# Kernel tuning notes

Hardware: AMD Instinct MI355X
Metric: run time of the kernel (lower is better)

## Reference

```python
import jax, jax.numpy as jnp
import numpy as np

N_HEAD = 8
HIDDEN = 512
EPS_LN = 1e-3  # keras LayerNormalization default epsilon


def layernorm(x, gamma, beta, eps=EPS_LN):
    mu = jnp.mean(x, axis=-1, keepdims=True)
    var = jnp.mean((x - mu) ** 2, axis=-1, keepdims=True)
    return (x - mu) * jax.lax.rsqrt(var + eps) * gamma + beta


def setup_inputs() -> dict:
    key = jax.random.key(0)
    ks = jax.random.split(key, 10)
    bs, NE, F = 512, 128, HIDDEN
    x = jax.random.normal(ks[0], (bs, NE, F), dtype=jnp.float32)
    mask = (jax.random.uniform(ks[1], (bs, 1, NE)) < 0.85).astype(jnp.float32)
    # guarantee at least one live entity per row
    mask = mask.at[:, :, 0].set(1.0)
    s = 1.0 / np.sqrt(F)
    Wqk = jax.random.normal(ks[2], (F, 2 * HIDDEN), dtype=jnp.float32) * s
    bqk = jnp.zeros((2 * HIDDEN,), jnp.float32)
    Wv = jax.random.normal(ks[3], (F, HIDDEN), dtype=jnp.float32) * s
    bv = jnp.zeros((HIDDEN,), jnp.float32)
    Wmlp = jax.random.normal(ks[4], (F, HIDDEN), dtype=jnp.float32) * s
    bmlp = jnp.zeros((HIDDEN,), jnp.float32)
    g_pre = jnp.ones((F,), jnp.float32)
    b_pre = jnp.zeros((F,), jnp.float32)
    g_post = jnp.ones((F,), jnp.float32)
    b_post = jnp.zeros((F,), jnp.float32)
    return dict(x=x, mask=mask, Wqk=Wqk, bqk=bqk, Wv=Wv, bv=bv,
                Wmlp=Wmlp, bmlp=bmlp, g_pre=g_pre, b_pre=b_pre,
                g_post=g_post, b_post=b_post)


def reference(x, mask, Wqk, bqk, Wv, bv, Wmlp, bmlp, g_pre, b_pre, g_post, b_post):
    bs, NE, F = x.shape
    h, d = N_HEAD, HIDDEN // N_HEAD
    x4 = x[:, None]  # (bs, 1, NE, F)

    # pre-norm only feeds qkv projections; residual uses raw x4
    inp = layernorm(x4, g_pre, b_pre)

    qk = (inp @ Wqk + bqk).reshape(bs, 1, NE, h, d, 2)
    q, k = qk[..., 0], qk[..., 1]                       # (bs,1,NE,h,d)
    v = (inp @ Wv + bv).reshape(bs, 1, NE, h, d)

    logits = jnp.einsum('btnhd,btmhd->bthnm', q, k) / np.sqrt(d)  # (bs,1,h,NE,NE)

    m5 = mask[:, :, None, None, :]                      # (bs,1,1,1,NE)
    logits = logits - (1.0 - m5) * 1e10
    logits = logits - jnp.max(logits, axis=-1, keepdims=True)
    un = jnp.exp(logits) * m5
    p = un / (jnp.sum(un, axis=-1, keepdims=True) + 1e-10)
    p = p * m5

    att = jnp.einsum('bthnm,btmhd->btnhd', p, v).reshape(bs, 1, NE, HIDDEN)
    a = att @ Wmlp + bmlp                               # mlp_layer=1, no activation
    y = x4 + a                                          # residual
    y = layernorm(y, g_post, b_post)

    # masked average pooling over entities
    mE = mask[..., None]                                # (bs,1,NE,1)
    pooled = jnp.sum(y * mE, axis=-2) / (jnp.sum(mE, axis=-2) + 1e-5)  # (bs,1,F)
    return pooled.reshape(bs, F)
```

## Files before the change

kernel.cpp:

```cpp
#include <hip/hip_runtime.h>
#include <hip/hip_bf16.h>


typedef __bf16 bf16;
typedef __bf16 bf16x8 __attribute__((ext_vector_type(8)));
typedef __bf16 bf16x4 __attribute__((ext_vector_type(4)));
typedef float f32x4 __attribute__((ext_vector_type(4)));

__device__ __forceinline__ f32x4 mfma16(bf16x8 a, bf16x8 b, f32x4 c) {
    return __builtin_amdgcn_mfma_f32_16x16x32_bf16(a, b, c, 0, 0, 0);
}

typedef const unsigned int __attribute__((address_space(1)))* gptr_t;
typedef unsigned int __attribute__((address_space(3)))* lptr_t;
__device__ __forceinline__ void gld16(const void* g, void* l) {
    __builtin_amdgcn_global_load_lds((gptr_t)g, (lptr_t)l, 16, 0, 0);
}

#define SWZ(byteoff, row) ((byteoff) ^ (((row) & 7) << 4))


__global__ __launch_bounds__(256) void prep_split_kernel(
    const float* __restrict__ Wqk, const float* __restrict__ bqk,
    const float* __restrict__ Wv, const float* __restrict__ bv,
    const float* __restrict__ Wmlp,
    bf16* __restrict__ Wqkv_s, bf16* __restrict__ Wmlp_s, float* __restrict__ bQKV)
{
    int t = blockIdx.x * 256 + threadIdx.x;
    if (t < 524288) {
        int k = t >> 10, c = t & 1023;
        int h = c >> 7, w7 = c & 127, d = w7 >> 1, isK = w7 & 1;
        int n = isK * 512 + h * 64 + d;
        int tn = n >> 7, nc = n & 127, kc = k >> 6, kw = k & 63;
        Wqkv_s[((size_t)(tn * 8 + kc) * 128 + nc) * 64 + kw] = (bf16)Wqk[t];
    } else if (t < 786432) {
        int u = t - 524288;
        int k = u >> 9, c = u & 511;
        int n = 1024 + c;
        int tn = n >> 7, nc = n & 127, kc = k >> 6, kw = k & 63;
        Wqkv_s[((size_t)(tn * 8 + kc) * 128 + nc) * 64 + kw] = (bf16)Wv[u];
    } else if (t < 1048576) {
        int u = t - 786432;
        int k = u >> 9, c = u & 511;
        int chunk = k >> 5, kw = k & 31;
        Wmlp_s[chunk * 16384 + c * 32 + (kw ^ ((c & 3) << 3))] = (bf16)Wmlp[u];
    } else if (t < 1050112) {
        int j = t - 1048576;
        int region = j >> 9, w9 = j & 511, h = w9 >> 6, d = w9 & 63;
        float v;
        if (region == 0)      v = bqk[h * 128 + d * 2];
        else if (region == 1) v = bqk[h * 128 + d * 2 + 1];
        else                  v = bv[h * 64 + d];
        bQKV[j] = v;
    }
}

__global__ __launch_bounds__(256) void ln_kernel(
    const float* __restrict__ x, const float* __restrict__ g,
    const float* __restrict__ b, bf16* __restrict__ inp)
{
    int row = blockIdx.x * 4 + (threadIdx.x >> 6);
    int lane = threadIdx.x & 63;
    int k0 = lane * 8;
    const float* xr = x + (size_t)row * 512 + k0;
    f32x4 a0 = *(const f32x4*)xr;
    f32x4 a1 = *(const f32x4*)(xr + 4);
    float s = 0.f, ss = 0.f;
#pragma unroll
    for (int i = 0; i < 4; i++) {
        s += a0[i] + a1[i];
        ss += a0[i] * a0[i] + a1[i] * a1[i];
    }
#pragma unroll
    for (int m = 1; m < 64; m <<= 1) {
        s  += __shfl_xor(s, m, 64);
        ss += __shfl_xor(ss, m, 64);
    }
    float mu = s * (1.f / 512.f);
    float rstd = rsqrtf(ss * (1.f / 512.f) - mu * mu + 1e-3f);
    f32x4 g0 = *(const f32x4*)(g + k0);
    f32x4 g1 = *(const f32x4*)(g + k0 + 4);
    f32x4 b0 = *(const f32x4*)(b + k0);
    f32x4 b1 = *(const f32x4*)(b + k0 + 4);
    bf16x8 ov;
#pragma unroll
    for (int i = 0; i < 4; i++) {
        ov[i]     = (bf16)((a0[i] - mu) * rstd * g0[i] + b0[i]);
        ov[i + 4] = (bf16)((a1[i] - mu) * rstd * g1[i] + b1[i]);
    }
    *(bf16x8*)(inp + (size_t)row * 512 + k0) = ov;
}

__global__ __launch_bounds__(256) void qkv_gemm_kernel(
    const bf16* __restrict__ inp, const bf16* __restrict__ Wqkv_s,
    const float* __restrict__ bQKV,
    bf16* __restrict__ q, bf16* __restrict__ kbuf, bf16* __restrict__ vt)
{
    __shared__ __align__(16) bf16 As[128 * 64];
    __shared__ __align__(16) bf16 Bs[128 * 64];
    const int bid = blockIdx.x;
    const int idx = (bid & 7) * 768 + (bid >> 3);
    const int tm = idx / 12, tn = idx % 12;
    const int tid = threadIdx.x;
    const int w = tid >> 6, l = tid & 63;
    const int wr = w >> 1, wc = w & 1;
    const int l15 = l & 15, l4 = l >> 4;

    const f32x4 fz = {0.f, 0.f, 0.f, 0.f};
    f32x4 acc[4][4];
#pragma unroll
    for (int m = 0; m < 4; m++)
#pragma unroll
        for (int n = 0; n < 4; n++) acc[m][n] = fz;

    const int arow = l >> 3;
    const int axc = ((l & 7) ^ arow) * 8;
    const bf16* Abase = inp + (size_t)(tm * 128) * 512;
    const int rsw = (l15 & 7) << 4;

    for (int kc = 0; kc < 8; kc++) {
#pragma unroll
        for (int i = 0; i < 4; i++) {
            int rg = (i * 4 + w) * 8;
            gld16(Abase + (size_t)(rg + arow) * 512 + kc * 64 + axc,
                  As + (i * 4 + w) * 512);
        }
        const bf16* Bbase = Wqkv_s + (size_t)(tn * 8 + kc) * 8192;
#pragma unroll
        for (int i = 0; i < 4; i++) {
            gld16(Bbase + (size_t)((i * 4 + w) * 8 + arow) * 64 + axc,
                  Bs + (i * 4 + w) * 512);
        }
        __syncthreads();
#pragma unroll
        for (int kk = 0; kk < 2; kk++) {
            const int kb = (kk * 64 + l4 * 16) ^ rsw;
            bf16x8 af[4], bfr[4];
#pragma unroll
            for (int m = 0; m < 4; m++)
                af[m] = *(const bf16x8*)((const char*)As + (wr * 64 + m * 16 + l15) * 128 + kb);
#pragma unroll
            for (int n = 0; n < 4; n++)
                bfr[n] = *(const bf16x8*)((const char*)Bs + (wc * 64 + n * 16 + l15) * 128 + kb);
#pragma unroll
            for (int m = 0; m < 4; m++)
#pragma unroll
                for (int n = 0; n < 4; n++)
                    acc[m][n] = mfma16(af[m], bfr[n], acc[m][n]);
        }
        __syncthreads();
    }

    const int colBase = tn * 128 + wc * 64;
    const int mrowBase = tm * 128 + wr * 64;
#pragma unroll
    for (int n = 0; n < 4; n++) {
        int col = colBase + n * 16 + l15;
        float bias = bQKV[col];
        int within = col & 511, hh = within >> 6, dd = within & 63;
#pragma unroll
        for (int m = 0; m < 4; m++) {
            int mr0 = mrowBase + m * 16 + l4 * 4;
            int bb = mr0 >> 7, e0 = mr0 & 127;
            size_t base = (size_t)(bb * 8 + hh) * 8192;
            if (tn < 4) {
#pragma unroll
                for (int r = 0; r < 4; r++)
                    q[base + (size_t)(e0 + r) * 64 + dd] = (bf16)(acc[m][n][r] + bias);
            } else if (tn < 8) {
#pragma unroll
                for (int r = 0; r < 4; r++) {
                    int e = e0 + r;
                    kbuf[base + (size_t)e * 64 + (dd ^ ((e & 7) << 3))] = (bf16)(acc[m][n][r] + bias);
                }
            } else {
                bf16x4 pk;
#pragma unroll
                for (int r = 0; r < 4; r++) pk[r] = (bf16)(acc[m][n][r] + bias);
                *(bf16x4*)(vt + base + (size_t)dd * 128 + (e0 ^ ((dd & 7) << 3))) = pk;
            }
        }
    }
}

__global__ __launch_bounds__(512) void attn_split_kernel(
    const bf16* __restrict__ q, const bf16* __restrict__ kbuf,
    const bf16* __restrict__ vt, const float* __restrict__ mask,
    bf16* __restrict__ att)
{
    __shared__ __align__(16) char Ks[128 * 128];
    __shared__ __align__(16) char VTs[64 * 256];
    __shared__ __align__(16) char Ps[128 * 256];
    __shared__ float mrow[128];

    const int bid = blockIdx.x;
    const int b = bid & 511, h = bid >> 9;
    const size_t bh = (size_t)(b * 8 + h);
    const int tid = threadIdx.x;
    const int w = tid >> 6, l = tid & 63;
    const int l15 = l & 15, l4 = l >> 4, R0 = w * 16;

    const bf16* kb = kbuf + bh * 8192;
    const bf16* vb = vt + bh * 8192;
#pragma unroll
    for (int i = 0; i < 2; i++) {
        gld16(kb + ((i * 8 + w) * 64 + l) * 8, (bf16*)Ks + (i * 8 + w) * 512);
        gld16(vb + ((i * 8 + w) * 64 + l) * 8, (bf16*)VTs + (i * 8 + w) * 512);
    }
    if (tid < 128) mrow[tid] = mask[b * 128 + tid];
    __syncthreads();

    const f32x4 fz = {0.f, 0.f, 0.f, 0.f};
    const bf16* qp = q + bh * 8192 + (size_t)(R0 + l15) * 64 + l4 * 8;
    bf16x8 af0 = *(const bf16x8*)(qp);
    bf16x8 af1 = *(const bf16x8*)(qp + 32);
    f32x4 accL[8];
#pragma unroll
    for (int n = 0; n < 8; n++) accL[n] = fz;
#pragma unroll
    for (int ks = 0; ks < 2; ks++) {
        bf16x8 af = ks ? af1 : af0;
        int k2 = (ks * 32 + l4 * 8) * 2;
#pragma unroll
        for (int nt = 0; nt < 8; nt++) {
            int krow = nt * 16 + l15;
            bf16x8 bfr = *(const bf16x8*)(Ks + krow * 128 + (k2 ^ ((krow & 7) << 4)));
            accL[nt] = mfma16(af, bfr, accL[nt]);
        }
    }
    float pv[32];
#pragma unroll
    for (int r = 0; r < 4; r++) {
        float mx = -1e30f;
#pragma unroll
        for (int nt = 0; nt < 8; nt++) {
            int colk = nt * 16 + l15;
            float v = accL[nt][r] * 0.125f - (1.0f - mrow[colk]) * 1e10f;
            pv[nt * 4 + r] = v;
            mx = fmaxf(mx, v);
        }
#pragma unroll
        for (int m = 1; m < 16; m <<= 1) mx = fmaxf(mx, __shfl_xor(mx, m, 64));
        float sum = 0.f;
#pragma unroll
        for (int nt = 0; nt < 8; nt++) {
            int colk = nt * 16 + l15;
            float e = __expf(pv[nt * 4 + r] - mx) * mrow[colk];
            pv[nt * 4 + r] = e;
            sum += e;
        }
#pragma unroll
        for (int m = 1; m < 16; m <<= 1) sum += __shfl_xor(sum, m, 64);
        float inv = 1.0f / (sum + 1e-10f);
        int prow = R0 + l4 * 4 + r;
#pragma unroll
        for (int nt = 0; nt < 8; nt++) {
            bf16 pb = (bf16)(pv[nt * 4 + r] * inv);
            *(bf16*)(Ps + prow * 256 + SWZ((nt * 16 + l15) * 2, prow)) = pb;
        }
    }
    __syncthreads();

    f32x4 accO[4];
#pragma unroll
    for (int n = 0; n < 4; n++) accO[n] = fz;
#pragma unroll
    for (int ks = 0; ks < 4; ks++) {
        int k2 = (ks * 32 + l4 * 8) * 2;
        int prow = R0 + l15;
        bf16x8 af = *(const bf16x8*)(Ps + prow * 256 + (k2 ^ ((prow & 7) << 4)));
#pragma unroll
        for (int nt = 0; nt < 4; nt++) {
            int d = nt * 16 + l15;
            bf16x8 bfr = *(const bf16x8*)(VTs + d * 256 + (k2 ^ ((d & 7) << 4)));
            accO[nt] = mfma16(af, bfr, accO[nt]);
        }
    }
    bf16* outp = att + (size_t)(b * 128) * 512 + h * 64;
#pragma unroll
    for (int nt = 0; nt < 4; nt++) {
        int d = nt * 16 + l15;
#pragma unroll
        for (int r = 0; r < 4; r++) {
            int e = R0 + l4 * 4 + r;
            outp[(size_t)e * 512 + d] = (bf16)accO[nt][r];
        }
    }
}

__global__ __launch_bounds__(512) void mlp_split_kernel(
    const bf16* __restrict__ att, const bf16* __restrict__ Wmlp_s,
    const float* __restrict__ bmlp, const float* __restrict__ x,
    const float* __restrict__ mask, const float* __restrict__ gpost,
    const float* __restrict__ bpost, float* __restrict__ out)
{
    __shared__ __align__(16) bf16 Bs[2][512 * 32];
    __shared__ float pool[512];
    __shared__ float gb[1024];
    __shared__ float mrow[128];
    __shared__ float msum_s;

    const int b = blockIdx.x;
    const int tid = threadIdx.x;
    const int w = tid >> 6, l = tid & 63;
    const int l15 = l & 15, l4 = l >> 4;
    const int R0 = w * 16;

    pool[tid] = 0.f;
    gb[tid] = gpost[tid];
    gb[512 + tid] = bpost[tid];
    if (tid < 128) mrow[tid] = mask[b * 128 + tid];

#pragma unroll
    for (int i = 0; i < 4; i++)
        gld16(Wmlp_s + ((i * 8 + w) * 64 + l) * 8, &Bs[0][(i * 8 + w) * 512]);
    __syncthreads();
    if (w == 0) {
        float v = mrow[l] + mrow[64 + l];
#pragma unroll
        for (int m = 1; m < 64; m <<= 1) v += __shfl_xor(v, m, 64);
        if (l == 0) msum_s = v;
    }

    const f32x4 fz = {0.f, 0.f, 0.f, 0.f};
    f32x4 acc[32];
#pragma unroll
    for (int n = 0; n < 32; n++) acc[n] = fz;
    const bf16* Ab = att + (size_t)(b * 128 + R0 + l15) * 512 + l4 * 8;
    int cur = 0;
    for (int ks = 0; ks < 16; ks++) {
        if (ks < 15) {
            const bf16* src = Wmlp_s + (ks + 1) * 16384;
#pragma unroll
            for (int i = 0; i < 4; i++)
                gld16(src + ((i * 8 + w) * 64 + l) * 8, &Bs[cur ^ 1][(i * 8 + w) * 512]);
        }
        bf16x8 af = *(const bf16x8*)(Ab + ks * 32);
#pragma unroll
        for (int nt = 0; nt < 32; nt++) {
            int ncol = nt * 16 + l15;
            bf16x8 bfr = *(const bf16x8*)((const char*)&Bs[cur][0] + ncol * 64 + ((l4 * 16) ^ ((ncol & 3) << 4)));
            acc[nt] = mfma16(af, bfr, acc[nt]);
        }
        __syncthreads();
        cur ^= 1;
    }
#pragma unroll
    for (int nt = 0; nt < 32; nt++) {
        int col = nt * 16 + l15;
        float bb = bmlp[col];
#pragma unroll
        for (int r = 0; r < 4; r++) {
            int row = R0 + l4 * 4 + r;
            acc[nt][r] = acc[nt][r] + bb + x[((size_t)b * 128 + row) * 512 + col];
        }
    }
    float mu[4], rs[4];
#pragma unroll
    for (int r = 0; r < 4; r++) {
        float s = 0.f, ss = 0.f;
#pragma unroll
        for (int nt = 0; nt < 32; nt++) {
            float v = acc[nt][r];
            s += v; ss += v * v;
        }
#pragma unroll
        for (int m = 1; m < 16; m <<= 1) {
            s  += __shfl_xor(s, m, 64);
            ss += __shfl_xor(ss, m, 64);
        }
        float m_ = s * (1.f / 512.f);
        mu[r] = m_;
        rs[r] = rsqrtf(ss * (1.f / 512.f) - m_ * m_ + 1e-3f);
    }
#pragma unroll
    for (int nt = 0; nt < 32; nt++) {
        int col = nt * 16 + l15;
        float g = gb[col], bb = gb[512 + col];
        float s = 0.f;
#pragma unroll
        for (int r = 0; r < 4; r++) {
            int row = R0 + l4 * 4 + r;
            float y = (acc[nt][r] - mu[r]) * rs[r] * g + bb;
            s += y * mrow[row];
        }
        atomicAdd(&pool[col], s);
    }
    __syncthreads();
    out[(size_t)b * 512 + tid] = pool[tid] / (msum_s + 1e-5f);
}

__global__ __launch_bounds__(256) void prep_kernel(
    const float* __restrict__ Wqk, const float* __restrict__ bqk,
    const float* __restrict__ Wv, const float* __restrict__ bv,
    const float* __restrict__ Wmlp,
    bf16* __restrict__ Wqkv_t, bf16* __restrict__ Wmlp_t, float* __restrict__ bQKV)
{
    int t = blockIdx.x * 256 + threadIdx.x;
    const int NQKV = 8 * 192 * 512;
    if (t < NQKV) {
        int h = t / (192 * 512);
        int rem = t - h * (192 * 512);
        int n = rem >> 9;
        int k = rem & 511;
        float v;
        if (n < 64)       v = Wqk[k * 1024 + h * 128 + n * 2];
        else if (n < 128) v = Wqk[k * 1024 + h * 128 + (n - 64) * 2 + 1];
        else              v = Wv[k * 512 + h * 64 + (n - 128)];
        Wqkv_t[t] = (bf16)v;
    } else {
        int u = t - NQKV;
        if (u < 512 * 512) {
            int col = u >> 9, k = u & 511;
            Wmlp_t[u] = (bf16)Wmlp[k * 512 + col];
        } else {
            int j = u - 512 * 512;
            if (j < 1536) {
                int h = j / 192, n = j - h * 192;
                float v;
                if (n < 64)       v = bqk[h * 128 + n * 2];
                else if (n < 128) v = bqk[h * 128 + (n - 64) * 2 + 1];
                else              v = bv[h * 64 + (n - 128)];
                bQKV[j] = v;
            }
        }
    }
}

__global__ __launch_bounds__(512) void attn_kernel(
    const bf16* __restrict__ inp, const float* __restrict__ mask,
    const bf16* __restrict__ Wqkv_t, const float* __restrict__ bQKV,
    bf16* __restrict__ att)
{
    __shared__ __align__(16) char Qs[128 * 128];
    __shared__ __align__(16) char Ks[128 * 128];
    __shared__ __align__(16) char VTs[64 * 256];
    __shared__ __align__(16) char Ps[128 * 256];
    __shared__ float mrow[128];

    const int bid = blockIdx.x;
    const int b = bid & 511;
    const int h = bid >> 9;
    const int tid = threadIdx.x;
    const int w = tid >> 6, l = tid & 63;
    const int l15 = l & 15, l4 = l >> 4;
    const int R0 = w * 16;

    if (tid < 128) mrow[tid] = mask[b * 128 + tid];

    const bf16* A  = inp + (size_t)(b * 128) * 512;
    const bf16* Wh = Wqkv_t + (size_t)h * 192 * 512;
    const f32x4 fz = {0.f, 0.f, 0.f, 0.f};

    f32x4 acc[12];
#pragma unroll
    for (int n = 0; n < 12; n++) acc[n] = fz;
    const bf16* aptr = A + (size_t)(R0 + l15) * 512 + l4 * 8;
#pragma unroll 4
    for (int ks = 0; ks < 16; ks++) {
        bf16x8 af = *(const bf16x8*)(aptr + ks * 32);
#pragma unroll
        for (int n = 0; n < 12; n++) {
            bf16x8 bfr = *(const bf16x8*)(Wh + (size_t)(n * 16 + l15) * 512 + ks * 32 + l4 * 8);
            acc[n] = mfma16(af, bfr, acc[n]);
        }
    }
#pragma unroll
    for (int n = 0; n < 12; n++) {
        int col = n * 16 + l15;
        float bias = bQKV[h * 192 + col];
#pragma unroll
        for (int r = 0; r < 4; r++) {
            int row = R0 + l4 * 4 + r;
            bf16 val = (bf16)(acc[n][r] + bias);
            if (n < 4) {
                *(bf16*)(Qs + row * 128 + SWZ(col * 2, row)) = val;
            } else if (n < 8) {
                *(bf16*)(Ks + row * 128 + SWZ((col - 64) * 2, row)) = val;
            } else {
                int d = col - 128;
                *(bf16*)(VTs + d * 256 + SWZ(row * 2, d)) = val;
            }
        }
    }
    __syncthreads();

    f32x4 accL[8];
#pragma unroll
    for (int n = 0; n < 8; n++) accL[n] = fz;
#pragma unroll
    for (int ks = 0; ks < 2; ks++) {
        int k = ks * 32 + l4 * 8;
        int qrow = R0 + l15;
        bf16x8 af = *(const bf16x8*)(Qs + qrow * 128 + SWZ(k * 2, qrow));
#pragma unroll
        for (int nt = 0; nt < 8; nt++) {
            int krow = nt * 16 + l15;
            bf16x8 bfr = *(const bf16x8*)(Ks + krow * 128 + SWZ(k * 2, krow));
            accL[nt] = mfma16(af, bfr, accL[nt]);
        }
    }
    float pv[32];
#pragma unroll
    for (int r = 0; r < 4; r++) {
        float mx = -1e30f;
#pragma unroll
        for (int nt = 0; nt < 8; nt++) {
            int colk = nt * 16 + l15;
            float v = accL[nt][r] * 0.125f - (1.0f - mrow[colk]) * 1e10f;
            pv[nt * 4 + r] = v;
            mx = fmaxf(mx, v);
        }
#pragma unroll
        for (int m = 1; m < 16; m <<= 1) mx = fmaxf(mx, __shfl_xor(mx, m, 64));
        float sum = 0.f;
#pragma unroll
        for (int nt = 0; nt < 8; nt++) {
            int colk = nt * 16 + l15;
            float e = __expf(pv[nt * 4 + r] - mx) * mrow[colk];
            pv[nt * 4 + r] = e;
            sum += e;
        }
#pragma unroll
        for (int m = 1; m < 16; m <<= 1) sum += __shfl_xor(sum, m, 64);
        float inv = 1.0f / (sum + 1e-10f);
        int prow = R0 + l4 * 4 + r;
#pragma unroll
        for (int nt = 0; nt < 8; nt++) {
            bf16 pb = (bf16)(pv[nt * 4 + r] * inv);
            *(bf16*)(Ps + prow * 256 + SWZ((nt * 16 + l15) * 2, prow)) = pb;
        }
    }
    __syncthreads();

    f32x4 accO[4];
#pragma unroll
    for (int n = 0; n < 4; n++) accO[n] = fz;
#pragma unroll
    for (int ks = 0; ks < 4; ks++) {
        int k = ks * 32 + l4 * 8;
        int prow = R0 + l15;
        bf16x8 af = *(const bf16x8*)(Ps + prow * 256 + SWZ(k * 2, prow));
#pragma unroll
        for (int nt = 0; nt < 4; nt++) {
            int d = nt * 16 + l15;
            bf16x8 bfr = *(const bf16x8*)(VTs + d * 256 + SWZ(k * 2, d));
            accO[nt] = mfma16(af, bfr, accO[nt]);
        }
    }
    bf16* outp = att + (size_t)(b * 128) * 512 + h * 64;
#pragma unroll
    for (int nt = 0; nt < 4; nt++) {
        int d = nt * 16 + l15;
#pragma unroll
        for (int r = 0; r < 4; r++) {
            int e = R0 + l4 * 4 + r;
            outp[(size_t)e * 512 + d] = (bf16)accO[nt][r];
        }
    }
}

__global__ __launch_bounds__(512) void mlp_kernel(
    const bf16* __restrict__ att, const bf16* __restrict__ Wmlp_t,
    const float* __restrict__ bmlp, const float* __restrict__ x,
    const float* __restrict__ mask, const float* __restrict__ gpost,
    const float* __restrict__ bpost, float* __restrict__ out)
{
    __shared__ float pool[512];
    __shared__ float gb[1024];
    __shared__ float mrow[128];
    __shared__ float msum_s;

    const int b = blockIdx.x;
    const int tid = threadIdx.x;
    const int w = tid >> 6, l = tid & 63;
    const int l15 = l & 15, l4 = l >> 4;
    const int R0 = w * 16;

    pool[tid] = 0.f;
    gb[tid] = gpost[tid];
    gb[512 + tid] = bpost[tid];
    if (tid < 128) mrow[tid] = mask[b * 128 + tid];
    __syncthreads();
    if (w == 0) {
        float v = mrow[l] + mrow[64 + l];
#pragma unroll
        for (int m = 1; m < 64; m <<= 1) v += __shfl_xor(v, m, 64);
        if (l == 0) msum_s = v;
    }

    const f32x4 fz = {0.f, 0.f, 0.f, 0.f};
    f32x4 acc[32];
#pragma unroll
    for (int n = 0; n < 32; n++) acc[n] = fz;
    const bf16* Ab = att + (size_t)(b * 128 + R0 + l15) * 512 + l4 * 8;
#pragma unroll 2
    for (int ks = 0; ks < 16; ks++) {
        bf16x8 af = *(const bf16x8*)(Ab + ks * 32);
#pragma unroll
        for (int nt = 0; nt < 32; nt++) {
            bf16x8 bfr = *(const bf16x8*)(Wmlp_t + (size_t)(nt * 16 + l15) * 512 + ks * 32 + l4 * 8);
            acc[nt] = mfma16(af, bfr, acc[nt]);
        }
    }
#pragma unroll
    for (int nt = 0; nt < 32; nt++) {
        int col = nt * 16 + l15;
        float bb = bmlp[col];
#pragma unroll
        for (int r = 0; r < 4; r++) {
            int row = R0 + l4 * 4 + r;
            acc[nt][r] = acc[nt][r] + bb + x[((size_t)b * 128 + row) * 512 + col];
        }
    }
    float mu[4], rs[4];
#pragma unroll
    for (int r = 0; r < 4; r++) {
        float s = 0.f, ss = 0.f;
#pragma unroll
        for (int nt = 0; nt < 32; nt++) {
            float v = acc[nt][r];
            s += v; ss += v * v;
        }
#pragma unroll
        for (int m = 1; m < 16; m <<= 1) {
            s  += __shfl_xor(s, m, 64);
            ss += __shfl_xor(ss, m, 64);
        }
        float m_ = s * (1.f / 512.f);
        mu[r] = m_;
        rs[r] = rsqrtf(ss * (1.f / 512.f) - m_ * m_ + 1e-3f);
    }
#pragma unroll
    for (int nt = 0; nt < 32; nt++) {
        int col = nt * 16 + l15;
        float g = gb[col], bb = gb[512 + col];
        float s = 0.f;
#pragma unroll
        for (int r = 0; r < 4; r++) {
            int row = R0 + l4 * 4 + r;
            float y = (acc[nt][r] - mu[r]) * rs[r] * g + bb;
            s += y * mrow[row];
        }
        atomicAdd(&pool[col], s);
    }
    __syncthreads();
    out[(size_t)b * 512 + tid] = pool[tid] / (msum_s + 1e-5f);
}

extern "C" void kernel_launch(void* const* d_in, const int* in_sizes, int n_in,
                              void* d_out, int out_size, void* d_ws, size_t ws_size,
                              hipStream_t stream)
{
    const float* x     = (const float*)d_in[0];
    const float* mask  = (const float*)d_in[1];
    const float* Wqk   = (const float*)d_in[2];
    const float* bqk   = (const float*)d_in[3];
    const float* Wv    = (const float*)d_in[4];
    const float* bv    = (const float*)d_in[5];
    const float* Wmlp  = (const float*)d_in[6];
    const float* bmlp  = (const float*)d_in[7];
    const float* gpre  = (const float*)d_in[8];
    const float* bpre  = (const float*)d_in[9];
    const float* gpost = (const float*)d_in[10];
    const float* bpost = (const float*)d_in[11];
    float* out = (float*)d_out;
    char* ws = (char*)d_ws;

    const size_t NEED_SPLIT = 270538752;
    if (ws_size >= NEED_SPLIT) {
        bf16*  q      = (bf16*)ws;
        bf16*  kbuf   = (bf16*)(ws + (size_t)67108864);
        bf16*  vt     = (bf16*)(ws + (size_t)134217728);
        bf16*  inp    = (bf16*)(ws + (size_t)201326592);
        bf16*  att    = inp;
        bf16*  Wqkv_s = (bf16*)(ws + (size_t)268435456);
        bf16*  Wmlp_s = (bf16*)(ws + (size_t)270008320);
        float* bQKV   = (float*)(ws + (size_t)270532608);

        prep_split_kernel<<<4103, 256, 0, stream>>>(Wqk, bqk, Wv, bv, Wmlp, Wqkv_s, Wmlp_s, bQKV);
        ln_kernel<<<16384, 256, 0, stream>>>(x, gpre, bpre, inp);
        qkv_gemm_kernel<<<6144, 256, 0, stream>>>(inp, Wqkv_s, bQKV, q, kbuf, vt);
        attn_split_kernel<<<4096, 512, 0, stream>>>(q, kbuf, vt, mask, att);
        mlp_split_kernel<<<512, 512, 0, stream>>>(att, Wmlp_s, bmlp, x, mask, gpost, bpost, out);
    } else {
        bf16*  inp    = (bf16*)ws;
        bf16*  att    = (bf16*)(ws + 67108864);
        bf16*  Wqkv_t = (bf16*)(ws + 134217728);
        bf16*  Wmlp_t = (bf16*)(ws + 134217728 + 1572864);
        float* bQKV   = (float*)(ws + 134217728 + 1572864 + 524288);

        prep_kernel<<<4103, 256, 0, stream>>>(Wqk, bqk, Wv, bv, Wmlp, Wqkv_t, Wmlp_t, bQKV);
        ln_kernel<<<16384, 256, 0, stream>>>(x, gpre, bpre, inp);
        attn_kernel<<<4096, 512, 0, stream>>>(inp, mask, Wqkv_t, bQKV, att);
        mlp_kernel<<<512, 512, 0, stream>>>(att, Wmlp_t, bmlp, x, mask, gpost, bpost, out);
    }
}
```

Baseline: 654.9 us.

## Split MLP into tiled GEMM kernel plus separate post-LN pooling kernel

```diff
diff --git a/kernel.cpp b/kernel.cpp
--- a/kernel.cpp
+++ b/kernel.cpp
@@ -24,7 +24,7 @@
     const float* __restrict__ Wqk, const float* __restrict__ bqk,
     const float* __restrict__ Wv, const float* __restrict__ bv,
     const float* __restrict__ Wmlp,
-    bf16* __restrict__ Wqkv_s, bf16* __restrict__ Wmlp_s, float* __restrict__ bQKV)
+    bf16* __restrict__ Wqkv_s, bf16* __restrict__ Wmlp_t, float* __restrict__ bQKV)
 {
     int t = blockIdx.x * 256 + threadIdx.x;
     if (t < 524288) {
@@ -42,8 +42,8 @@
     } else if (t < 1048576) {
         int u = t - 786432;
         int k = u >> 9, c = u & 511;
-        int chunk = k >> 5, kw = k & 31;
-        Wmlp_s[chunk * 16384 + c * 32 + (kw ^ ((c & 3) << 3))] = (bf16)Wmlp[u];
+        int tn = c >> 7, nc = c & 127, kc = k >> 6, kw = k & 63;
+        Wmlp_t[((size_t)(tn * 8 + kc) * 128 + nc) * 64 + kw] = (bf16)Wmlp[u];
     } else if (t < 1050112) {
         int j = t - 1048576;
         int region = j >> 9, w9 = j & 511, h = w9 >> 6, d = w9 & 63;
@@ -288,32 +288,96 @@
     }
 }
 
-__global__ __launch_bounds__(512) void mlp_split_kernel(
-    const bf16* __restrict__ att, const bf16* __restrict__ Wmlp_s,
-    const float* __restrict__ bmlp, const float* __restrict__ x,
+__global__ __launch_bounds__(256) void mlp_gemm_kernel(
+    const bf16* __restrict__ att, const bf16* __restrict__ Wmlp_t,
+    const float* __restrict__ bmlp, float* __restrict__ y)
+{
+    __shared__ __align__(16) bf16 As[128 * 64];
+    __shared__ __align__(16) bf16 Bs[128 * 64];
+    const int bid = blockIdx.x;
+    const int idx = (bid & 7) * 256 + (bid >> 3);
+    const int tm = idx >> 2, tn = idx & 3;
+    const int tid = threadIdx.x;
+    const int w = tid >> 6, l = tid & 63;
+    const int wr = w >> 1, wc = w & 1;
+    const int l15 = l & 15, l4 = l >> 4;
+
+    const f32x4 fz = {0.f, 0.f, 0.f, 0.f};
+    f32x4 acc[4][4];
+#pragma unroll
+    for (int m = 0; m < 4; m++)
+#pragma unroll
+        for (int n = 0; n < 4; n++) acc[m][n] = fz;
+
+    const int arow = l >> 3;
+    const int axc = ((l & 7) ^ arow) * 8;
+    const bf16* Abase = att + (size_t)(tm * 128) * 512;
+    const int rsw = (l15 & 7) << 4;
+
+    for (int kc = 0; kc < 8; kc++) {
+#pragma unroll
+        for (int i = 0; i < 4; i++) {
+            int rg = (i * 4 + w) * 8;
+            gld16(Abase + (size_t)(rg + arow) * 512 + kc * 64 + axc,
+                  As + (i * 4 + w) * 512);
+        }
+        const bf16* Bbase = Wmlp_t + (size_t)(tn * 8 + kc) * 8192;
+#pragma unroll
+        for (int i = 0; i < 4; i++) {
+            gld16(Bbase + (size_t)((i * 4 + w) * 8 + arow) * 64 + axc,
+                  Bs + (i * 4 + w) * 512);
+        }
+        __syncthreads();
+#pragma unroll
+        for (int kk = 0; kk < 2; kk++) {
+            const int kb = (kk * 64 + l4 * 16) ^ rsw;
+            bf16x8 af[4], bfr[4];
+#pragma unroll
+            for (int m = 0; m < 4; m++)
+                af[m] = *(const bf16x8*)((const char*)As + (wr * 64 + m * 16 + l15) * 128 + kb);
+#pragma unroll
+            for (int n = 0; n < 4; n++)
+                bfr[n] = *(const bf16x8*)((const char*)Bs + (wc * 64 + n * 16 + l15) * 128 + kb);
+#pragma unroll
+            for (int m = 0; m < 4; m++)
+#pragma unroll
+                for (int n = 0; n < 4; n++)
+                    acc[m][n] = mfma16(af[m], bfr[n], acc[m][n]);
+        }
+        __syncthreads();
+    }
+
+    const int colBase = tn * 128 + wc * 64;
+    const int mrowBase = tm * 128 + wr * 64;
+#pragma unroll
+    for (int n = 0; n < 4; n++) {
+        int col = colBase + n * 16 + l15;
+        float bias = bmlp[col];
+#pragma unroll
+        for (int m = 0; m < 4; m++) {
+            int row0 = mrowBase + m * 16 + l4 * 4;
+#pragma unroll
+            for (int r = 0; r < 4; r++)
+                y[(size_t)(row0 + r) * 512 + col] = acc[m][n][r] + bias;
+        }
+    }
+}
+
+__global__ __launch_bounds__(512) void pool_kernel(
+    const float* __restrict__ y, const float* __restrict__ x,
     const float* __restrict__ mask, const float* __restrict__ gpost,
     const float* __restrict__ bpost, float* __restrict__ out)
 {
-    __shared__ __align__(16) bf16 Bs[2][512 * 32];
-    __shared__ float pool[512];
-    __shared__ float gb[1024];
+    __shared__ float partial[8][512];
     __shared__ float mrow[128];
     __shared__ float msum_s;
 
     const int b = blockIdx.x;
     const int tid = threadIdx.x;
     const int w = tid >> 6, l = tid & 63;
-    const int l15 = l & 15, l4 = l >> 4;
-    const int R0 = w * 16;
-
-    pool[tid] = 0.f;
-    gb[tid] = gpost[tid];
-    gb[512 + tid] = bpost[tid];
+    const int k0 = l * 8;
+
     if (tid < 128) mrow[tid] = mask[b * 128 + tid];
-
-#pragma unroll
-    for (int i = 0; i < 4; i++)
-        gld16(Wmlp_s + ((i * 8 + w) * 64 + l) * 8, &Bs[0][(i * 8 + w) * 512]);
     __syncthreads();
     if (w == 0) {
         float v = mrow[l] + mrow[64 + l];
@@ -322,72 +386,48 @@
         if (l == 0) msum_s = v;
     }
 
-    const f32x4 fz = {0.f, 0.f, 0.f, 0.f};
-    f32x4 acc[32];
-#pragma unroll
-    for (int n = 0; n < 32; n++) acc[n] = fz;
-    const bf16* Ab = att + (size_t)(b * 128 + R0 + l15) * 512 + l4 * 8;
-    int cur = 0;
-    for (int ks = 0; ks < 16; ks++) {
-        if (ks < 15) {
-            const bf16* src = Wmlp_s + (ks + 1) * 16384;
-#pragma unroll
-            for (int i = 0; i < 4; i++)
-                gld16(src + ((i * 8 + w) * 64 + l) * 8, &Bs[cur ^ 1][(i * 8 + w) * 512]);
-        }
-        bf16x8 af = *(const bf16x8*)(Ab + ks * 32);
-#pragma unroll
-        for (int nt = 0; nt < 32; nt++) {
-            int ncol = nt * 16 + l15;
-            bf16x8 bfr = *(const bf16x8*)((const char*)&Bs[cur][0] + ncol * 64 + ((l4 * 16) ^ ((ncol & 3) << 4)));
-            acc[nt] = mfma16(af, bfr, acc[nt]);
-        }
-        __syncthreads();
-        cur ^= 1;
-    }
-#pragma unroll
-    for (int nt = 0; nt < 32; nt++) {
-        int col = nt * 16 + l15;
-        float bb = bmlp[col];
-#pragma unroll
-        for (int r = 0; r < 4; r++) {
-            int row = R0 + l4 * 4 + r;
-            acc[nt][r] = acc[nt][r] + bb + x[((size_t)b * 128 + row) * 512 + col];
-        }
-    }
-    float mu[4], rs[4];
-#pragma unroll
-    for (int r = 0; r < 4; r++) {
+    f32x4 g0 = *(const f32x4*)(gpost + k0);
+    f32x4 g1 = *(const f32x4*)(gpost + k0 + 4);
+    f32x4 b0 = *(const f32x4*)(bpost + k0);
+    f32x4 b1 = *(const f32x4*)(bpost + k0 + 4);
+
+    f32x4 a0 = {0.f, 0.f, 0.f, 0.f}, a1 = {0.f, 0.f, 0.f, 0.f};
+    for (int i = 0; i < 16; i++) {
+        int row = w * 16 + i;
+        const float* yr = y + ((size_t)(b * 128 + row)) * 512 + k0;
+        const float* xr = x + ((size_t)(b * 128 + row)) * 512 + k0;
+        f32x4 v0 = *(const f32x4*)yr + *(const f32x4*)xr;
+        f32x4 v1 = *(const f32x4*)(yr + 4) + *(const f32x4*)(xr + 4);
         float s = 0.f, ss = 0.f;
 #pragma unroll
-        for (int nt = 0; nt < 32; nt++) {
-            float v = acc[nt][r];
-            s += v; ss += v * v;
-        }
-#pragma unroll
-        for (int m = 1; m < 16; m <<= 1) {
+        for (int j = 0; j < 4; j++) {
+            s += v0[j] + v1[j];
+            ss += v0[j] * v0[j] + v1[j] * v1[j];
+        }
+#pragma unroll
+        for (int m = 1; m < 64; m <<= 1) {
             s  += __shfl_xor(s, m, 64);
             ss += __shfl_xor(ss, m, 64);
         }
-        float m_ = s * (1.f / 512.f);
-        mu[r] = m_;
-        rs[r] = rsqrtf(ss * (1.f / 512.f) - m_ * m_ + 1e-3f);
-    }
-#pragma unroll
-    for (int nt = 0; nt < 32; nt++) {
-        int col = nt * 16 + l15;
-        float g = gb[col], bb = gb[512 + col];
-        float s = 0.f;
-#pragma unroll
-        for (int r = 0; r < 4; r++) {
-            int row = R0 + l4 * 4 + r;
-            float y = (acc[nt][r] - mu[r]) * rs[r] * g + bb;
-            s += y * mrow[row];
-        }
-        atomicAdd(&pool[col], s);
+        float mu = s * (1.f / 512.f);
+        float rstd = rsqrtf(ss * (1.f / 512.f) - mu * mu + 1e-3f);
+        float mr = mrow[row];
+#pragma unroll
+        for (int j = 0; j < 4; j++) {
+            a0[j] += ((v0[j] - mu) * rstd * g0[j] + b0[j]) * mr;
+            a1[j] += ((v1[j] - mu) * rstd * g1[j] + b1[j]) * mr;
+        }
+    }
+#pragma unroll
+    for (int j = 0; j < 4; j++) {
+        partial[w][k0 + j]     = a0[j];
+        partial[w][k0 + 4 + j] = a1[j];
     }
     __syncthreads();
-    out[(size_t)b * 512 + tid] = pool[tid] / (msum_s + 1e-5f);
+    float t = 0.f;
+#pragma unroll
+    for (int ww = 0; ww < 8; ww++) t += partial[ww][tid];
+    out[(size_t)b * 512 + tid] = t / (msum_s + 1e-5f);
 }
 
 __global__ __launch_bounds__(256) void prep_kernel(
@@ -674,15 +714,17 @@
         bf16*  vt     = (bf16*)(ws + (size_t)134217728);
         bf16*  inp    = (bf16*)(ws + (size_t)201326592);
         bf16*  att    = inp;
+        float* y      = (float*)ws;
         bf16*  Wqkv_s = (bf16*)(ws + (size_t)268435456);
-        bf16*  Wmlp_s = (bf16*)(ws + (size_t)270008320);
+        bf16*  Wmlp_t = (bf16*)(ws + (size_t)270008320);
         float* bQKV   = (float*)(ws + (size_t)270532608);
 
-        prep_split_kernel<<<4103, 256, 0, stream>>>(Wqk, bqk, Wv, bv, Wmlp, Wqkv_s, Wmlp_s, bQKV);
+        prep_split_kernel<<<4103, 256, 0, stream>>>(Wqk, bqk, Wv, bv, Wmlp, Wqkv_s, Wmlp_t, bQKV);
         ln_kernel<<<16384, 256, 0, stream>>>(x, gpre, bpre, inp);
         qkv_gemm_kernel<<<6144, 256, 0, stream>>>(inp, Wqkv_s, bQKV, q, kbuf, vt);
         attn_split_kernel<<<4096, 512, 0, stream>>>(q, kbuf, vt, mask, att);
-        mlp_split_kernel<<<512, 512, 0, stream>>>(att, Wmlp_s, bmlp, x, mask, gpost, bpost, out);
+        mlp_gemm_kernel<<<2048, 256, 0, stream>>>(att, Wmlp_t, bmlp, y);
+        pool_kernel<<<512, 512, 0, stream>>>(y, x, mask, gpost, bpost, out);
     } else {
         bf16*  inp    = (bf16*)ws;
         bf16*  att    = (bf16*)(ws + 67108864);
```

Result: faster. 556.7 us (-15.0%).
